# Kernel tuning notes

Measured on AMD Instinct MI355X. Metric: run time of the kernel, lower is better.

Reference implementation:

```python
import jax, jax.numpy as jnp
import numpy as np

N = 100000        # num_nodes
W_IN = 256        # input feature dim
W_OUT = 64        # args.node_dim
C = 2             # args.num_channels
T = 4             # num_edge_type
E = 800000        # edges per edge type
NUM_CLASS = 4
M = 20000         # number of target nodes
BETA = 0.5        # args.beta


def setup_inputs() -> dict:
    key = jax.random.key(0)
    ks = jax.random.split(key, 10)
    X = jax.random.normal(ks[0], (N, W_IN), dtype=jnp.float32)
    edge_index = jax.random.randint(ks[1], (T, 2, E), 0, N)
    edge_value = jax.random.uniform(ks[2], (T, E), dtype=jnp.float32)
    target_x = jax.random.randint(ks[3], (M,), 0, N)
    target = jax.random.randint(ks[4], (M,), 0, NUM_CLASS)
    # learned params
    Ws = jax.random.normal(ks[5], (C, W_IN, W_OUT), dtype=jnp.float32) * 0.05   # GCNConv weights
    conv_weight = jax.random.normal(ks[6], (C, T), dtype=jnp.float32) * 0.1     # FastGTConv.weight
    linear1_W = jax.random.normal(ks[7], (W_OUT, W_OUT * C), dtype=jnp.float32) * 0.05
    linear1_b = jnp.zeros((W_OUT,), dtype=jnp.float32)
    lin_W = jax.random.normal(ks[8], (NUM_CLASS, W_OUT), dtype=jnp.float32) * 0.05
    lin_b = jnp.zeros((NUM_CLASS,), dtype=jnp.float32)
    return dict(X=X, edge_value=edge_value, Ws=Ws, conv_weight=conv_weight,
                linear1_W=linear1_W, linear1_b=linear1_b, lin_W=lin_W, lin_b=lin_b,
                edge_index=edge_index, target_x=target_x, target=target)


def reference(X, edge_value, Ws, conv_weight, linear1_W, linear1_b, lin_W, lin_b,
              edge_index, target_x, target):
    # FastGTConv: softmax over edge types per channel
    filt = jax.nn.softmax(conv_weight, axis=1)            # [C, T]
    rows = edge_index[:, 0, :].reshape(-1)                # [T*E]
    cols = edge_index[:, 1, :].reshape(-1)                # [T*E]
    # X_ = H = [X @ W_c for each channel]
    X_ = jnp.einsum('nd,cdo->cno', X, Ws)                 # [C, N, W_OUT]
    outs = []
    for c in range(C):
        # concat+coalesce(add) then spmm == scatter-add of weighted messages
        vals = (edge_value * filt[c][:, None]).reshape(-1)       # [T*E]
        msgs = vals[:, None] * X_[c][cols]                        # [T*E, W_OUT]
        Hc = jax.ops.segment_sum(msgs, rows, num_segments=N)      # [N, W_OUT]
        outs.append(jax.nn.relu(BETA * X_[c] + (1.0 - BETA) * Hc))
    H_ = jnp.concatenate(outs, axis=1)                    # [N, C*W_OUT]
    H_ = jax.nn.relu(H_ @ linear1_W.T + linear1_b)        # [N, W_OUT]
    y = H_[target_x] @ lin_W.T + lin_b                    # [M, NUM_CLASS]
    logp = jax.nn.log_softmax(y, axis=-1)
    loss = -jnp.mean(jnp.take_along_axis(logp, target[:, None], axis=1))
    return loss, y
```

## Files before the change

kernel.cpp:

```cpp
#include <hip/hip_runtime.h>

#define N_NODES 100000
#define W_INF   256
#define W_OUTF  64
#define C_CH    2
#define T_ET    4
#define E_EDGE  800000
#define NUM_CLS 4
#define M_TGT   20000
#define BETA    0.5f
#define MAXDEG  96

typedef __attribute__((ext_vector_type(8))) short bf16x8;
typedef __attribute__((ext_vector_type(4))) float floatx4;

__device__ inline short f2bf(float f) {
    unsigned u = __builtin_bit_cast(unsigned, f);
    u += 0x7FFF + ((u >> 16) & 1);
    return (short)(u >> 16);
}

__global__ void setup_kernel(const float* __restrict__ Ws,
                             const float* __restrict__ conv_weight,
                             const int* __restrict__ target_x,
                             short* __restrict__ Bt, float* __restrict__ filt,
                             int* __restrict__ rid, int* __restrict__ nrows,
                             float* __restrict__ out) {
    int i = blockIdx.x * 256 + threadIdx.x;
    if (i == 0) { *nrows = 0; out[0] = 0.f; }
    if (i < C_CH) {
        int c = i;
        float mx = -1e30f;
        for (int t = 0; t < T_ET; t++) mx = fmaxf(mx, conv_weight[c * T_ET + t]);
        float e[T_ET];
        float s = 0.f;
        for (int t = 0; t < T_ET; t++) { e[t] = expf(conv_weight[c * T_ET + t] - mx); s += e[t]; }
        for (int t = 0; t < T_ET; t++) filt[c * T_ET + t] = e[t] / s;
    }
    if (i < C_CH * W_OUTF * W_INF) {
        int co = i >> 8, k = i & 255;
        int c = co >> 6, o = co & 63;
        Bt[i] = f2bf(Ws[((size_t)c * W_INF + k) * W_OUTF + o]);
    }
    if (i < M_TGT) rid[target_x[i]] = -2;
}

__global__ void compact_kernel(int* __restrict__ rid, int* __restrict__ row_list,
                               int* __restrict__ nrows, int* __restrict__ counts) {
    int n = blockIdx.x * blockDim.x + threadIdx.x;
    if (n < M_TGT) counts[n] = 0;
    int lane = threadIdx.x & 63;
    bool flag = (n < N_NODES) && (rid[n] == -2);
    unsigned long long mask = __ballot(flag);
    int base = 0;
    if (lane == 0 && mask) base = atomicAdd(nrows, __popcll(mask));
    base = __shfl(base, 0);
    if (flag) {
        int id = base + __popcll(mask & ((1ULL << lane) - 1ULL));
        rid[n] = id;
        row_list[id] = n;
    }
}

__global__ void build_kernel(const int* __restrict__ edge_index,
                             const float* __restrict__ edge_value,
                             const int* __restrict__ rid,
                             int* __restrict__ counts,
                             unsigned long long* __restrict__ records) {
    int t = blockIdx.y;
    int i = blockIdx.x * 256 + threadIdx.x;
    if (i >= E_EDGE / 8) return;
    int e = i * 8;
    const int*   rbase = &edge_index[(size_t)(t * 2 + 0) * E_EDGE + e];
    const int*   cbase = &edge_index[(size_t)(t * 2 + 1) * E_EDGE + e];
    const float* vbase = &edge_value[(size_t)t * E_EDGE + e];
    int4   r4a = *(const int4*)  &rbase[0], r4b = *(const int4*)  &rbase[4];
    int4   c4a = *(const int4*)  &cbase[0], c4b = *(const int4*)  &cbase[4];
    float4 v4a = *(const float4*)&vbase[0], v4b = *(const float4*)&vbase[4];
    int rows[8] = {r4a.x, r4a.y, r4a.z, r4a.w, r4b.x, r4b.y, r4b.z, r4b.w};
    int cols[8] = {c4a.x, c4a.y, c4a.z, c4a.w, c4b.x, c4b.y, c4b.z, c4b.w};
    float evv[8] = {v4a.x, v4a.y, v4a.z, v4a.w, v4b.x, v4b.y, v4b.z, v4b.w};
    int ids[8];
    #pragma unroll
    for (int j = 0; j < 8; j++) ids[j] = rid[rows[j]];
    #pragma unroll
    for (int j = 0; j < 8; j++) {
        if (ids[j] >= 0) {
            int p = atomicAdd(&counts[ids[j]], 1);
            if (p < MAXDEG) {
                unsigned long long rec =
                    (unsigned long long)(unsigned)(cols[j] | (t << 20)) |
                    ((unsigned long long)__float_as_uint(evv[j]) << 32);
                records[(size_t)ids[j] * MAXDEG + p] = rec;
            }
        }
    }
}

#define GMT  64
#define BLDA 264
__global__ __launch_bounds__(256, 4)
void gemm_mfma_kernel(const float* __restrict__ X, const short* __restrict__ Bt,
                      float* __restrict__ Xp) {
    __shared__ short Bl[64][BLDA];
    int tid = threadIdx.x;
    int w = tid >> 6, lane = tid & 63;
    int quad = lane >> 4, l15 = lane & 15;
    int m0 = blockIdx.x * GMT + w * 16;
    int arow = m0 + l15;
    if (arow >= N_NODES) arow = N_NODES - 1;
    const float* xrow = X + (size_t)arow * W_INF;
    bf16x8 af[8];
    #pragma unroll
    for (int kc = 0; kc < 8; kc++) {
        int kb = kc * 32 + quad * 8;
        float4 v0 = *(const float4*)&xrow[kb];
        float4 v1 = *(const float4*)&xrow[kb + 4];
        af[kc][0] = f2bf(v0.x); af[kc][1] = f2bf(v0.y);
        af[kc][2] = f2bf(v0.z); af[kc][3] = f2bf(v0.w);
        af[kc][4] = f2bf(v1.x); af[kc][5] = f2bf(v1.y);
        af[kc][6] = f2bf(v1.z); af[kc][7] = f2bf(v1.w);
    }
    floatx4 acc[C_CH][4] = {};
    for (int c = 0; c < C_CH; c++) {
        if (c) __syncthreads();
        #pragma unroll
        for (int l = 0; l < 8; l++) {
            int idx = tid + l * 256;
            int r = idx >> 5;
            int kp = (idx & 31) * 8;
            *(bf16x8*)&Bl[r][kp] = *(const bf16x8*)&Bt[(size_t)(c * 64 + r) * W_INF + kp];
        }
        __syncthreads();
        #pragma unroll
        for (int kc = 0; kc < 8; kc++) {
            int kb = kc * 32 + quad * 8;
            #pragma unroll
            for (int nt = 0; nt < 4; nt++) {
                bf16x8 b = *(bf16x8*)&Bl[nt * 16 + l15][kb];
                acc[c][nt] = __builtin_amdgcn_mfma_f32_16x16x32_bf16(af[kc], b, acc[c][nt], 0, 0, 0);
            }
        }
    }
    #pragma unroll
    for (int c = 0; c < C_CH; c++) {
        #pragma unroll
        for (int nt = 0; nt < 4; nt++) {
            int o = nt * 16 + l15;
            #pragma unroll
            for (int r = 0; r < 4; r++) {
                int m = m0 + quad * 4 + r;
                if (m < N_NODES)
                    Xp[((size_t)c * N_NODES + m) * W_OUTF + o] = acc[c][nt][r];
            }
        }
    }
}

__global__ void gather_kernel(const int* __restrict__ row_list,
                              const int* __restrict__ counts,
                              const unsigned long long* __restrict__ records,
                              const float* __restrict__ filt,
                              const float* __restrict__ Xp,
                              float* __restrict__ Hcat,
                              const int* __restrict__ nrows_ptr) {
    int b = blockIdx.x;
    if (b >= *nrows_ptr) return;
    int c = threadIdx.x >> 6, lane = threadIdx.x & 63;
    float f[T_ET];
    #pragma unroll
    for (int t = 0; t < T_ET; t++) f[t] = filt[c * T_ET + t];
    int n = row_list[b];
    int cnt = counts[b]; if (cnt > MAXDEG) cnt = MAXDEG;
    const unsigned long long* rec = records + (size_t)b * MAXDEG;
    const float* xb = Xp + (size_t)c * N_NODES * W_OUTF + lane;
    float acc = 0.f;
    int p = 0;
    for (; p + 3 < cnt; p += 4) {
        unsigned long long r0 = rec[p],     r1 = rec[p + 1];
        unsigned long long r2 = rec[p + 2], r3 = rec[p + 3];
        int k0 = (int)(unsigned)r0, k1 = (int)(unsigned)r1;
        int k2 = (int)(unsigned)r2, k3 = (int)(unsigned)r3;
        float e0 = __uint_as_float((unsigned)(r0 >> 32));
        float e1 = __uint_as_float((unsigned)(r1 >> 32));
        float e2 = __uint_as_float((unsigned)(r2 >> 32));
        float e3 = __uint_as_float((unsigned)(r3 >> 32));
        float x0 = xb[(size_t)(k0 & 0xFFFFF) * W_OUTF];
        float x1 = xb[(size_t)(k1 & 0xFFFFF) * W_OUTF];
        float x2 = xb[(size_t)(k2 & 0xFFFFF) * W_OUTF];
        float x3 = xb[(size_t)(k3 & 0xFFFFF) * W_OUTF];
        acc += e0 * f[k0 >> 20] * x0 + e1 * f[k1 >> 20] * x1
             + e2 * f[k2 >> 20] * x2 + e3 * f[k3 >> 20] * x3;
    }
    for (; p < cnt; p++) {
        unsigned long long r0 = rec[p];
        int k0 = (int)(unsigned)r0;
        float e0 = __uint_as_float((unsigned)(r0 >> 32));
        acc += e0 * f[k0 >> 20] * xb[(size_t)(k0 & 0xFFFFF) * W_OUTF];
    }
    float xp = xb[(size_t)n * W_OUTF];
    float v = BETA * xp + (1.f - BETA) * acc;
    Hcat[(size_t)b * (C_CH * W_OUTF) + c * W_OUTF + lane] = fmaxf(v, 0.f);
}

#define HTGT 16
__global__ void head_kernel(const float* __restrict__ Hcat,
                            const int* __restrict__ rid,
                            const float* __restrict__ W1,
                            const float* __restrict__ b1,
                            const float* __restrict__ linW,
                            const float* __restrict__ linb,
                            const int* __restrict__ target_x,
                            const int* __restrict__ target,
                            float* __restrict__ out) {
    __shared__ float w1s[C_CH * W_OUTF][W_OUTF + 1];
    __shared__ float hcat_s[4][C_CH * W_OUTF];
    __shared__ float loss_s[4];
    int tid = threadIdx.x;
    for (int i = tid; i < W_OUTF * C_CH * W_OUTF; i += 256) {
        int o = i >> 7, k = i & 127;
        w1s[k][o] = W1[i];
    }
    int wave = tid >> 6, lane = tid & 63;
    float l0 = linW[0 * W_OUTF + lane], l1 = linW[1 * W_OUTF + lane];
    float l2 = linW[2 * W_OUTF + lane], l3 = linW[3 * W_OUTF + lane];
    float lb0 = linb[0], lb1 = linb[1], lb2 = linb[2], lb3 = linb[3];
    float bias = b1[lane];
    float lsum = 0.f;
    __syncthreads();
    for (int it = 0; it < HTGT / 4; it++) {
        int m = blockIdx.x * HTGT + it * 4 + wave;
        int row = target_x[m];
        int id = rid[row];
        hcat_s[wave][lane]      = Hcat[(size_t)id * (C_CH * W_OUTF) + lane];
        hcat_s[wave][64 + lane] = Hcat[(size_t)id * (C_CH * W_OUTF) + 64 + lane];
        __syncthreads();
        float acc = bias;
        #pragma unroll 8
        for (int k = 0; k < C_CH * W_OUTF; k++) acc += hcat_s[wave][k] * w1s[k][lane];
        float h2 = fmaxf(acc, 0.f);
        float p0 = l0 * h2, p1 = l1 * h2, p2 = l2 * h2, p3 = l3 * h2;
        #pragma unroll
        for (int off = 32; off > 0; off >>= 1) {
            p0 += __shfl_xor(p0, off);
            p1 += __shfl_xor(p1, off);
            p2 += __shfl_xor(p2, off);
            p3 += __shfl_xor(p3, off);
        }
        if (lane == 0) {
            float y[NUM_CLS];
            y[0] = p0 + lb0; y[1] = p1 + lb1; y[2] = p2 + lb2; y[3] = p3 + lb3;
            float mx = fmaxf(fmaxf(y[0], y[1]), fmaxf(y[2], y[3]));
            float s = 0.f;
            #pragma unroll
            for (int k = 0; k < NUM_CLS; k++) s += expf(y[k] - mx);
            float lse = mx + logf(s);
            #pragma unroll
            for (int k = 0; k < NUM_CLS; k++) out[1 + (size_t)m * NUM_CLS + k] = y[k];
            int tg = target[m];
            lsum += lse - y[tg];
        }
        __syncthreads();
    }
    if (lane == 0) loss_s[wave] = lsum;
    __syncthreads();
    if (tid == 0) {
        float L = loss_s[0] + loss_s[1] + loss_s[2] + loss_s[3];
        atomicAdd(&out[0], L * (1.0f / (float)M_TGT));
    }
}

extern "C" void kernel_launch(void* const* d_in, const int* in_sizes, int n_in,
                              void* d_out, int out_size, void* d_ws, size_t ws_size,
                              hipStream_t stream) {
    const float* X           = (const float*)d_in[0];
    const float* edge_value  = (const float*)d_in[1];
    const float* Ws          = (const float*)d_in[2];
    const float* conv_weight = (const float*)d_in[3];
    const float* linear1_W   = (const float*)d_in[4];
    const float* linear1_b   = (const float*)d_in[5];
    const float* lin_W       = (const float*)d_in[6];
    const float* lin_b       = (const float*)d_in[7];
    const int*   edge_index  = (const int*)d_in[8];
    const int*   target_x    = (const int*)d_in[9];
    const int*   target      = (const int*)d_in[10];
    float* out = (float*)d_out;

    char* ws = (char*)d_ws;
    size_t off = 0;
    float* filt  = (float*)(ws + off); off += 256;
    size_t xbytes = (size_t)C_CH * N_NODES * W_OUTF * sizeof(float);
    float* Xp    = (float*)(ws + off); off += xbytes;
    float* Hcat  = (float*)(ws + off); off += (size_t)M_TGT * C_CH * W_OUTF * sizeof(float);
    unsigned long long* records = (unsigned long long*)(ws + off);
    off += (size_t)M_TGT * MAXDEG * sizeof(unsigned long long);
    short* Bt    = (short*)(ws + off); off += (size_t)C_CH * W_OUTF * W_INF * sizeof(short);
    int*   rid   = (int*)  (ws + off); off += (size_t)N_NODES * sizeof(int);
    int*   row_list = (int*)(ws + off); off += (size_t)M_TGT * sizeof(int);
    int*   counts   = (int*)(ws + off); off += (size_t)M_TGT * sizeof(int);
    int*   nrows    = (int*)(ws + off); off += 256;

    hipMemsetAsync(rid, 0xFF, (size_t)N_NODES * sizeof(int), stream);

    setup_kernel<<<128, 256, 0, stream>>>(Ws, conv_weight, target_x, Bt, filt, rid, nrows, out);
    compact_kernel<<<(N_NODES + 255) / 256, 256, 0, stream>>>(rid, row_list, nrows, counts);
    dim3 bgrid((E_EDGE / 8 + 255) / 256, T_ET);
    build_kernel<<<bgrid, 256, 0, stream>>>(edge_index, edge_value, rid, counts, records);
    gemm_mfma_kernel<<<(N_NODES + GMT - 1) / GMT, 256, 0, stream>>>(X, Bt, Xp);
    gather_kernel<<<M_TGT, 128, 0, stream>>>(row_list, counts, records, filt, Xp, Hcat, nrows);
    head_kernel<<<M_TGT / HTGT, 256, 0, stream>>>(Hcat, rid, linear1_W, linear1_b, lin_W, lin_b,
                                                  target_x, target, out);
}
```

Baseline: 342.0 us.

## Fuse GEMM with edge build, store projected features as interleaved bf16

```diff
diff --git a/kernel.cpp b/kernel.cpp
--- a/kernel.cpp
+++ b/kernel.cpp
@@ -19,6 +19,8 @@
     u += 0x7FFF + ((u >> 16) & 1);
     return (short)(u >> 16);
 }
+__device__ inline float bflo(unsigned q) { return __builtin_bit_cast(float, q << 16); }
+__device__ inline float bfhi(unsigned q) { return __builtin_bit_cast(float, q & 0xFFFF0000u); }
 
 __global__ void setup_kernel(const float* __restrict__ Ws,
                              const float* __restrict__ conv_weight,
@@ -62,96 +64,100 @@
     }
 }
 
-__global__ void build_kernel(const int* __restrict__ edge_index,
-                             const float* __restrict__ edge_value,
-                             const int* __restrict__ rid,
-                             int* __restrict__ counts,
-                             unsigned long long* __restrict__ records) {
-    int t = blockIdx.y;
-    int i = blockIdx.x * 256 + threadIdx.x;
-    if (i >= E_EDGE / 8) return;
-    int e = i * 8;
-    const int*   rbase = &edge_index[(size_t)(t * 2 + 0) * E_EDGE + e];
-    const int*   cbase = &edge_index[(size_t)(t * 2 + 1) * E_EDGE + e];
-    const float* vbase = &edge_value[(size_t)t * E_EDGE + e];
-    int4   r4a = *(const int4*)  &rbase[0], r4b = *(const int4*)  &rbase[4];
-    int4   c4a = *(const int4*)  &cbase[0], c4b = *(const int4*)  &cbase[4];
-    float4 v4a = *(const float4*)&vbase[0], v4b = *(const float4*)&vbase[4];
-    int rows[8] = {r4a.x, r4a.y, r4a.z, r4a.w, r4b.x, r4b.y, r4b.z, r4b.w};
-    int cols[8] = {c4a.x, c4a.y, c4a.z, c4a.w, c4b.x, c4b.y, c4b.z, c4b.w};
-    float evv[8] = {v4a.x, v4a.y, v4a.z, v4a.w, v4b.x, v4b.y, v4b.z, v4b.w};
-    int ids[8];
-    #pragma unroll
-    for (int j = 0; j < 8; j++) ids[j] = rid[rows[j]];
-    #pragma unroll
-    for (int j = 0; j < 8; j++) {
-        if (ids[j] >= 0) {
-            int p = atomicAdd(&counts[ids[j]], 1);
-            if (p < MAXDEG) {
-                unsigned long long rec =
-                    (unsigned long long)(unsigned)(cols[j] | (t << 20)) |
-                    ((unsigned long long)__float_as_uint(evv[j]) << 32);
-                records[(size_t)ids[j] * MAXDEG + p] = rec;
-            }
-        }
-    }
-}
-
 #define GMT  64
 #define BLDA 264
+#define GEMM_NB  ((N_NODES + GMT - 1) / GMT)
+#define BUILD_BX ((E_EDGE / 8 + 255) / 256)
 __global__ __launch_bounds__(256, 4)
-void gemm_mfma_kernel(const float* __restrict__ X, const short* __restrict__ Bt,
-                      float* __restrict__ Xp) {
+void fused_gemm_build(const float* __restrict__ X, const short* __restrict__ Bt,
+                      short* __restrict__ Xp,
+                      const int* __restrict__ edge_index,
+                      const float* __restrict__ edge_value,
+                      const int* __restrict__ rid,
+                      int* __restrict__ counts,
+                      unsigned long long* __restrict__ records) {
     __shared__ short Bl[64][BLDA];
     int tid = threadIdx.x;
-    int w = tid >> 6, lane = tid & 63;
-    int quad = lane >> 4, l15 = lane & 15;
-    int m0 = blockIdx.x * GMT + w * 16;
-    int arow = m0 + l15;
-    if (arow >= N_NODES) arow = N_NODES - 1;
-    const float* xrow = X + (size_t)arow * W_INF;
-    bf16x8 af[8];
-    #pragma unroll
-    for (int kc = 0; kc < 8; kc++) {
-        int kb = kc * 32 + quad * 8;
-        float4 v0 = *(const float4*)&xrow[kb];
-        float4 v1 = *(const float4*)&xrow[kb + 4];
-        af[kc][0] = f2bf(v0.x); af[kc][1] = f2bf(v0.y);
-        af[kc][2] = f2bf(v0.z); af[kc][3] = f2bf(v0.w);
-        af[kc][4] = f2bf(v1.x); af[kc][5] = f2bf(v1.y);
-        af[kc][6] = f2bf(v1.z); af[kc][7] = f2bf(v1.w);
-    }
-    floatx4 acc[C_CH][4] = {};
-    for (int c = 0; c < C_CH; c++) {
-        if (c) __syncthreads();
-        #pragma unroll
-        for (int l = 0; l < 8; l++) {
-            int idx = tid + l * 256;
-            int r = idx >> 5;
-            int kp = (idx & 31) * 8;
-            *(bf16x8*)&Bl[r][kp] = *(const bf16x8*)&Bt[(size_t)(c * 64 + r) * W_INF + kp];
-        }
-        __syncthreads();
+    if (blockIdx.x < GEMM_NB) {
+        int w = tid >> 6, lane = tid & 63;
+        int quad = lane >> 4, l15 = lane & 15;
+        int m0 = blockIdx.x * GMT + w * 16;
+        int arow = m0 + l15;
+        if (arow >= N_NODES) arow = N_NODES - 1;
+        const float* xrow = X + (size_t)arow * W_INF;
+        bf16x8 af[8];
         #pragma unroll
         for (int kc = 0; kc < 8; kc++) {
             int kb = kc * 32 + quad * 8;
-            #pragma unroll
-            for (int nt = 0; nt < 4; nt++) {
-                bf16x8 b = *(bf16x8*)&Bl[nt * 16 + l15][kb];
-                acc[c][nt] = __builtin_amdgcn_mfma_f32_16x16x32_bf16(af[kc], b, acc[c][nt], 0, 0, 0);
+            float4 v0 = *(const float4*)&xrow[kb];
+            float4 v1 = *(const float4*)&xrow[kb + 4];
+            af[kc][0] = f2bf(v0.x); af[kc][1] = f2bf(v0.y);
+            af[kc][2] = f2bf(v0.z); af[kc][3] = f2bf(v0.w);
+            af[kc][4] = f2bf(v1.x); af[kc][5] = f2bf(v1.y);
+            af[kc][6] = f2bf(v1.z); af[kc][7] = f2bf(v1.w);
+        }
+        floatx4 acc[C_CH][4] = {};
+        for (int c = 0; c < C_CH; c++) {
+            if (c) __syncthreads();
+            #pragma unroll
+            for (int l = 0; l < 8; l++) {
+                int idx = tid + l * 256;
+                int r = idx >> 5;
+                int kp = (idx & 31) * 8;
+                *(bf16x8*)&Bl[r][kp] = *(const bf16x8*)&Bt[(size_t)(c * 64 + r) * W_INF + kp];
             }
-        }
-    }
-    #pragma unroll
-    for (int c = 0; c < C_CH; c++) {
+            __syncthreads();
+            #pragma unroll
+            for (int kc = 0; kc < 8; kc++) {
+                int kb = kc * 32 + quad * 8;
+                #pragma unroll
+                for (int nt = 0; nt < 4; nt++) {
+                    bf16x8 b = *(bf16x8*)&Bl[nt * 16 + l15][kb];
+                    acc[c][nt] = __builtin_amdgcn_mfma_f32_16x16x32_bf16(af[kc], b, acc[c][nt], 0, 0, 0);
+                }
+            }
+        }
         #pragma unroll
         for (int nt = 0; nt < 4; nt++) {
             int o = nt * 16 + l15;
             #pragma unroll
             for (int r = 0; r < 4; r++) {
                 int m = m0 + quad * 4 + r;
-                if (m < N_NODES)
-                    Xp[((size_t)c * N_NODES + m) * W_OUTF + o] = acc[c][nt][r];
+                if (m < N_NODES) {
+                    unsigned pk = (unsigned)(unsigned short)f2bf(acc[0][nt][r])
+                                | ((unsigned)(unsigned short)f2bf(acc[1][nt][r]) << 16);
+                    *(unsigned*)&Xp[(size_t)m * (C_CH * W_OUTF) + o * 2] = pk;
+                }
+            }
+        }
+    } else {
+        int bb = blockIdx.x - GEMM_NB;
+        int t = bb / BUILD_BX;
+        int i = (bb - t * BUILD_BX) * 256 + tid;
+        if (i >= E_EDGE / 8) return;
+        int e = i * 8;
+        const int*   rbase = &edge_index[(size_t)(t * 2 + 0) * E_EDGE + e];
+        const int*   cbase = &edge_index[(size_t)(t * 2 + 1) * E_EDGE + e];
+        const float* vbase = &edge_value[(size_t)t * E_EDGE + e];
+        int4   r4a = *(const int4*)  &rbase[0], r4b = *(const int4*)  &rbase[4];
+        int4   c4a = *(const int4*)  &cbase[0], c4b = *(const int4*)  &cbase[4];
+        float4 v4a = *(const float4*)&vbase[0], v4b = *(const float4*)&vbase[4];
+        int rows[8] = {r4a.x, r4a.y, r4a.z, r4a.w, r4b.x, r4b.y, r4b.z, r4b.w};
+        int cols[8] = {c4a.x, c4a.y, c4a.z, c4a.w, c4b.x, c4b.y, c4b.z, c4b.w};
+        float evv[8] = {v4a.x, v4a.y, v4a.z, v4a.w, v4b.x, v4b.y, v4b.z, v4b.w};
+        int ids[8];
+        #pragma unroll
+        for (int j = 0; j < 8; j++) ids[j] = rid[rows[j]];
+        #pragma unroll
+        for (int j = 0; j < 8; j++) {
+            if (ids[j] >= 0) {
+                int p = atomicAdd(&counts[ids[j]], 1);
+                if (p < MAXDEG) {
+                    unsigned long long rec =
+                        (unsigned long long)(unsigned)(cols[j] | (t << 20)) |
+                        ((unsigned long long)__float_as_uint(evv[j]) << 32);
+                    records[(size_t)ids[j] * MAXDEG + p] = rec;
+                }
             }
         }
     }
@@ -161,20 +167,20 @@
                               const int* __restrict__ counts,
                               const unsigned long long* __restrict__ records,
                               const float* __restrict__ filt,
-                              const float* __restrict__ Xp,
+                              const short* __restrict__ Xp,
                               float* __restrict__ Hcat,
                               const int* __restrict__ nrows_ptr) {
-    int b = blockIdx.x;
+    int w = threadIdx.x >> 6, lane = threadIdx.x & 63;
+    int b = blockIdx.x * 4 + w;
     if (b >= *nrows_ptr) return;
-    int c = threadIdx.x >> 6, lane = threadIdx.x & 63;
-    float f[T_ET];
+    float f0[T_ET], f1[T_ET];
     #pragma unroll
-    for (int t = 0; t < T_ET; t++) f[t] = filt[c * T_ET + t];
+    for (int t = 0; t < T_ET; t++) { f0[t] = filt[t]; f1[t] = filt[T_ET + t]; }
     int n = row_list[b];
     int cnt = counts[b]; if (cnt > MAXDEG) cnt = MAXDEG;
     const unsigned long long* rec = records + (size_t)b * MAXDEG;
-    const float* xb = Xp + (size_t)c * N_NODES * W_OUTF + lane;
-    float acc = 0.f;
+    const unsigned* xb = (const unsigned*)Xp + lane;
+    float a0 = 0.f, a1 = 0.f;
     int p = 0;
     for (; p + 3 < cnt; p += 4) {
         unsigned long long r0 = rec[p],     r1 = rec[p + 1];
@@ -185,22 +191,30 @@
         float e1 = __uint_as_float((unsigned)(r1 >> 32));
         float e2 = __uint_as_float((unsigned)(r2 >> 32));
         float e3 = __uint_as_float((unsigned)(r3 >> 32));
-        float x0 = xb[(size_t)(k0 & 0xFFFFF) * W_OUTF];
-        float x1 = xb[(size_t)(k1 & 0xFFFFF) * W_OUTF];
-        float x2 = xb[(size_t)(k2 & 0xFFFFF) * W_OUTF];
-        float x3 = xb[(size_t)(k3 & 0xFFFFF) * W_OUTF];
-        acc += e0 * f[k0 >> 20] * x0 + e1 * f[k1 >> 20] * x1
-             + e2 * f[k2 >> 20] * x2 + e3 * f[k3 >> 20] * x3;
+        unsigned q0 = xb[(size_t)(k0 & 0xFFFFF) * 64];
+        unsigned q1 = xb[(size_t)(k1 & 0xFFFFF) * 64];
+        unsigned q2 = xb[(size_t)(k2 & 0xFFFFF) * 64];
+        unsigned q3 = xb[(size_t)(k3 & 0xFFFFF) * 64];
+        int t0 = k0 >> 20, t1 = k1 >> 20, t2 = k2 >> 20, t3 = k3 >> 20;
+        a0 += e0 * f0[t0] * bflo(q0) + e1 * f0[t1] * bflo(q1)
+            + e2 * f0[t2] * bflo(q2) + e3 * f0[t3] * bflo(q3);
+        a1 += e0 * f1[t0] * bfhi(q0) + e1 * f1[t1] * bfhi(q1)
+            + e2 * f1[t2] * bfhi(q2) + e3 * f1[t3] * bfhi(q3);
     }
     for (; p < cnt; p++) {
         unsigned long long r0 = rec[p];
         int k0 = (int)(unsigned)r0;
         float e0 = __uint_as_float((unsigned)(r0 >> 32));
-        acc += e0 * f[k0 >> 20] * xb[(size_t)(k0 & 0xFFFFF) * W_OUTF];
-    }
-    float xp = xb[(size_t)n * W_OUTF];
-    float v = BETA * xp + (1.f - BETA) * acc;
-    Hcat[(size_t)b * (C_CH * W_OUTF) + c * W_OUTF + lane] = fmaxf(v, 0.f);
+        unsigned q0 = xb[(size_t)(k0 & 0xFFFFF) * 64];
+        int t0 = k0 >> 20;
+        a0 += e0 * f0[t0] * bflo(q0);
+        a1 += e0 * f1[t0] * bfhi(q0);
+    }
+    unsigned qn = xb[(size_t)n * 64];
+    float h0 = BETA * bflo(qn) + (1.f - BETA) * a0;
+    float h1 = BETA * bfhi(qn) + (1.f - BETA) * a1;
+    Hcat[(size_t)b * (C_CH * W_OUTF) + lane]          = fmaxf(h0, 0.f);
+    Hcat[(size_t)b * (C_CH * W_OUTF) + W_OUTF + lane] = fmaxf(h1, 0.f);
 }
 
 #define HTGT 16
@@ -289,8 +303,8 @@
     char* ws = (char*)d_ws;
     size_t off = 0;
     float* filt  = (float*)(ws + off); off += 256;
-    size_t xbytes = (size_t)C_CH * N_NODES * W_OUTF * sizeof(float);
-    float* Xp    = (float*)(ws + off); off += xbytes;
+    size_t xbytes = (size_t)N_NODES * C_CH * W_OUTF * sizeof(short);
+    short* Xp    = (short*)(ws + off); off += xbytes;
     float* Hcat  = (float*)(ws + off); off += (size_t)M_TGT * C_CH * W_OUTF * sizeof(float);
     unsigned long long* records = (unsigned long long*)(ws + off);
     off += (size_t)M_TGT * MAXDEG * sizeof(unsigned long long);
@@ -304,10 +318,9 @@
 
     setup_kernel<<<128, 256, 0, stream>>>(Ws, conv_weight, target_x, Bt, filt, rid, nrows, out);
     compact_kernel<<<(N_NODES + 255) / 256, 256, 0, stream>>>(rid, row_list, nrows, counts);
-    dim3 bgrid((E_EDGE / 8 + 255) / 256, T_ET);
-    build_kernel<<<bgrid, 256, 0, stream>>>(edge_index, edge_value, rid, counts, records);
-    gemm_mfma_kernel<<<(N_NODES + GMT - 1) / GMT, 256, 0, stream>>>(X, Bt, Xp);
-    gather_kernel<<<M_TGT, 128, 0, stream>>>(row_list, counts, records, filt, Xp, Hcat, nrows);
+    fused_gemm_build<<<GEMM_NB + BUILD_BX * T_ET, 256, 0, stream>>>(
+        X, Bt, Xp, edge_index, edge_value, rid, counts, records);
+    gather_kernel<<<(M_TGT + 3) / 4, 256, 0, stream>>>(row_list, counts, records, filt, Xp, Hcat, nrows);
     head_kernel<<<M_TGT / HTGT, 256, 0, stream>>>(Hcat, rid, linear1_W, linear1_b, lin_W, lin_b,
                                                   target_x, target, out);
 }
```

New measurement: 313.6 us. 8.3% less time.
